# Kernel tuning notes

Measured on AMD Instinct MI355X. Metric: run time of the kernel, lower is better.

Reference implementation:

```python
import jax, jax.numpy as jnp
import numpy as np

BINS = 10

def setup_inputs() -> dict:
    key = jax.random.key(0)
    k1, k2 = jax.random.split(key)
    N, C = 131072, 1000
    pred = jax.random.normal(k1, (N, C), dtype=jnp.float32)
    target = jax.random.randint(k2, (N,), 0, C, dtype=jnp.int64)
    return {"pred": pred, "target": target}


def reference(pred, target):
    # edges = [0, 0.1, ..., 1.0]; last edge nudged so values_clip == 1.0 lands in last bin
    edges = jnp.arange(BINS + 1, dtype=pred.dtype) / BINS
    edges = edges.at[-1].add(1e-6)

    N = pred.shape[0]
    # per-sample cross entropy: -log_softmax(pred)[i, target[i]]
    log_probs = jax.nn.log_softmax(pred, axis=-1)          # [N, C]
    values = -jnp.take_along_axis(log_probs, target[:, None], axis=-1)[:, 0]  # [N]

    # detached, normalized gradient-magnitude proxy in [0, 1]
    values_clip = jax.lax.stop_gradient(values)
    values_clip = values_clip / jnp.max(values_clip)

    # histogram binning: inds = (vc >= edges[i]) & (vc < edges[i+1])
    bin_idx = jnp.searchsorted(edges, values_clip, side='right') - 1
    bin_idx = jnp.clip(bin_idx, 0, BINS - 1)
    counts = jnp.zeros((BINS,), dtype=pred.dtype).at[bin_idx].add(1.0)

    n_nonempty = jnp.sum(counts > 0).astype(pred.dtype)
    tot = jnp.asarray(N, dtype=pred.dtype)

    # weight per bin = tot / num_in_bin for occupied bins (empty bins never indexed)
    per_bin_w = tot / jnp.where(counts > 0, counts, 1.0)
    weights = per_bin_w[bin_idx] / jnp.maximum(n_nonempty, 1.0) / tot
    weights = jax.lax.stop_gradient(weights)

    return jnp.sum(weights * values)
```

## Files before the change

kernel.cpp:

```cpp
#include <hip/hip_runtime.h>

#define N_SAMPLES 131072
#define N_CLASSES 1000
#define BINS 10


__global__ __launch_bounds__(256) void values_kernel(const float* __restrict__ pred,
                                                     const int* __restrict__ target,
                                                     float* __restrict__ values) {
    const int wave = threadIdx.x >> 6;
    const int lane = threadIdx.x & 63;
    const int row = blockIdx.x * 4 + wave;
    if (row >= N_SAMPLES) return;

    const float4* __restrict__ rp = (const float4*)(pred + (size_t)row * N_CLASSES);

    float4 r0 = rp[lane];
    float4 r1 = rp[64 + lane];
    float4 r2 = rp[128 + lane];
    const int i3 = (192 + lane < 250) ? (192 + lane) : 249;
    float4 r3 = rp[i3];

    const int t = target[row];
    const float xt = pred[(size_t)row * N_CLASSES + t];

    const bool v3 = (192 + lane) < 250;
    const float NEG_INF = -INFINITY;
    float r3x = v3 ? r3.x : NEG_INF;
    float r3y = v3 ? r3.y : NEG_INF;
    float r3z = v3 ? r3.z : NEG_INF;
    float r3w = v3 ? r3.w : NEG_INF;

    float m0 = fmaxf(fmaxf(r0.x, r0.y), fmaxf(r0.z, r0.w));
    float m1 = fmaxf(fmaxf(r1.x, r1.y), fmaxf(r1.z, r1.w));
    float m2 = fmaxf(fmaxf(r2.x, r2.y), fmaxf(r2.z, r2.w));
    float m3 = fmaxf(fmaxf(r3x, r3y), fmaxf(r3z, r3w));
    float lmax = fmaxf(fmaxf(m0, m1), fmaxf(m2, m3));
#pragma unroll
    for (int off = 32; off > 0; off >>= 1)
        lmax = fmaxf(lmax, __shfl_xor(lmax, off, 64));

    float s0 = __expf(r0.x - lmax) + __expf(r0.y - lmax) +
               __expf(r0.z - lmax) + __expf(r0.w - lmax);
    float s1 = __expf(r1.x - lmax) + __expf(r1.y - lmax) +
               __expf(r1.z - lmax) + __expf(r1.w - lmax);
    float s2 = __expf(r2.x - lmax) + __expf(r2.y - lmax) +
               __expf(r2.z - lmax) + __expf(r2.w - lmax);
    float s3 = __expf(r3x - lmax) + __expf(r3y - lmax) +
               __expf(r3z - lmax) + __expf(r3w - lmax);
    float s = (s0 + s1) + (s2 + s3);
#pragma unroll
    for (int off = 32; off > 0; off >>= 1)
        s += __shfl_xor(s, off, 64);

    if (lane == 0)
        values[row] = logf(s) + lmax - xt;
}

__global__ __launch_bounds__(256) void max_kernel(const float* __restrict__ values,
                                                  unsigned int* __restrict__ vmax_bits) {
    __shared__ float smax[4];
    float m = 0.f;
    for (int i = blockIdx.x * blockDim.x + threadIdx.x; i < N_SAMPLES;
         i += gridDim.x * blockDim.x)
        m = fmaxf(m, values[i]);
#pragma unroll
    for (int off = 32; off > 0; off >>= 1)
        m = fmaxf(m, __shfl_xor(m, off, 64));
    if ((threadIdx.x & 63) == 0) smax[threadIdx.x >> 6] = m;
    __syncthreads();
    if (threadIdx.x == 0) {
        float bm = fmaxf(fmaxf(smax[0], smax[1]), fmaxf(smax[2], smax[3]));
        atomicMax(vmax_bits, __float_as_uint(bm));
    }
}

__global__ __launch_bounds__(256) void hist_kernel(const float* __restrict__ values,
                                                   const unsigned int* __restrict__ vmax_bits,
                                                   unsigned int* __restrict__ counts,
                                                   float* __restrict__ sums) {
    __shared__ unsigned int lc[BINS];
    __shared__ float ls[BINS];
    if (threadIdx.x < BINS) { lc[threadIdx.x] = 0u; ls[threadIdx.x] = 0.f; }
    __syncthreads();

    const float vmax = __uint_as_float(*vmax_bits);
    float edges[BINS + 1];
#pragma unroll
    for (int j = 0; j <= BINS; ++j) edges[j] = (float)j / 10.0f;
    edges[BINS] += 1e-6f;

    for (int i = blockIdx.x * blockDim.x + threadIdx.x; i < N_SAMPLES;
         i += gridDim.x * blockDim.x) {
        float v = values[i];
        float vc = v / vmax;
        int bin = -1;
#pragma unroll
        for (int j = 0; j <= BINS; ++j) bin += (edges[j] <= vc) ? 1 : 0;
        bin = min(max(bin, 0), BINS - 1);
        atomicAdd(&lc[bin], 1u);
        atomicAdd(&ls[bin], v);
    }
    __syncthreads();
    if (threadIdx.x < BINS) {
        if (lc[threadIdx.x]) {
            atomicAdd(&counts[threadIdx.x], lc[threadIdx.x]);
            atomicAdd(&sums[threadIdx.x], ls[threadIdx.x]);
        }
    }
}

__global__ void final_kernel(const unsigned int* __restrict__ counts,
                             const float* __restrict__ sums,
                             float* __restrict__ out) {
    if (threadIdx.x == 0 && blockIdx.x == 0) {
        int nn = 0;
        float acc = 0.f;
#pragma unroll
        for (int b = 0; b < BINS; ++b) {
            unsigned int c = counts[b];
            if (c > 0u) { ++nn; acc += sums[b] / (float)c; }
        }
        float nne = (nn > 0) ? (float)nn : 1.f;
        out[0] = acc / nne;
    }
}

extern "C" void kernel_launch(void* const* d_in, const int* in_sizes, int n_in,
                              void* d_out, int out_size, void* d_ws, size_t ws_size,
                              hipStream_t stream) {
    const float* pred = (const float*)d_in[0];
    const int* target = (const int*)d_in[1];
    float* out = (float*)d_out;

    float* values = (float*)d_ws;
    unsigned int* stats = (unsigned int*)((char*)d_ws + (size_t)N_SAMPLES * sizeof(float));
    unsigned int* counts = stats + 1;
    float* sums = (float*)(stats + 11);

    hipMemsetAsync(stats, 0, 21 * sizeof(unsigned int), stream);

    values_kernel<<<N_SAMPLES / 4, 256, 0, stream>>>(pred, target, values);
    max_kernel<<<256, 256, 0, stream>>>(values, stats);
    hist_kernel<<<256, 256, 0, stream>>>(values, stats, counts, sums);
    final_kernel<<<1, 64, 0, stream>>>(counts, sums, out);
}
```

Measured before the change: 669.2 us.

## Fuse max reduction into values kernel and finalize in last hist block

```diff
diff --git a/kernel.cpp b/kernel.cpp
--- a/kernel.cpp
+++ b/kernel.cpp
@@ -7,11 +7,12 @@
 
 __global__ __launch_bounds__(256) void values_kernel(const float* __restrict__ pred,
                                                      const int* __restrict__ target,
-                                                     float* __restrict__ values) {
+                                                     float* __restrict__ values,
+                                                     unsigned int* __restrict__ vmax_bits) {
+    __shared__ float smax[4];
     const int wave = threadIdx.x >> 6;
     const int lane = threadIdx.x & 63;
     const int row = blockIdx.x * 4 + wave;
-    if (row >= N_SAMPLES) return;
 
     const float4* __restrict__ rp = (const float4*)(pred + (size_t)row * N_CLASSES);
 
@@ -53,21 +54,11 @@
     for (int off = 32; off > 0; off >>= 1)
         s += __shfl_xor(s, off, 64);
 
-    if (lane == 0)
-        values[row] = logf(s) + lmax - xt;
-}
-
-__global__ __launch_bounds__(256) void max_kernel(const float* __restrict__ values,
-                                                  unsigned int* __restrict__ vmax_bits) {
-    __shared__ float smax[4];
-    float m = 0.f;
-    for (int i = blockIdx.x * blockDim.x + threadIdx.x; i < N_SAMPLES;
-         i += gridDim.x * blockDim.x)
-        m = fmaxf(m, values[i]);
-#pragma unroll
-    for (int off = 32; off > 0; off >>= 1)
-        m = fmaxf(m, __shfl_xor(m, off, 64));
-    if ((threadIdx.x & 63) == 0) smax[threadIdx.x >> 6] = m;
+    if (lane == 0) {
+        float val = logf(s) + lmax - xt;
+        values[row] = val;
+        smax[wave] = val;
+    }
     __syncthreads();
     if (threadIdx.x == 0) {
         float bm = fmaxf(fmaxf(smax[0], smax[1]), fmaxf(smax[2], smax[3]));
@@ -78,9 +69,12 @@
 __global__ __launch_bounds__(256) void hist_kernel(const float* __restrict__ values,
                                                    const unsigned int* __restrict__ vmax_bits,
                                                    unsigned int* __restrict__ counts,
-                                                   float* __restrict__ sums) {
+                                                   float* __restrict__ sums,
+                                                   unsigned int* __restrict__ done,
+                                                   float* __restrict__ out) {
     __shared__ unsigned int lc[BINS];
     __shared__ float ls[BINS];
+    __shared__ bool amLast;
     if (threadIdx.x < BINS) { lc[threadIdx.x] = 0u; ls[threadIdx.x] = 0.f; }
     __syncthreads();
 
@@ -108,18 +102,23 @@
             atomicAdd(&sums[threadIdx.x], ls[threadIdx.x]);
         }
     }
-}
 
-__global__ void final_kernel(const unsigned int* __restrict__ counts,
-                             const float* __restrict__ sums,
-                             float* __restrict__ out) {
-    if (threadIdx.x == 0 && blockIdx.x == 0) {
+    __syncthreads();
+    if (threadIdx.x == 0) {
+        __threadfence();
+        unsigned int ticket = atomicAdd(done, 1u);
+        amLast = (ticket == gridDim.x - 1);
+    }
+    __syncthreads();
+    if (amLast && threadIdx.x == 0) {
+        __threadfence();
         int nn = 0;
         float acc = 0.f;
 #pragma unroll
         for (int b = 0; b < BINS; ++b) {
-            unsigned int c = counts[b];
-            if (c > 0u) { ++nn; acc += sums[b] / (float)c; }
+            unsigned int c = atomicAdd(&counts[b], 0u);
+            float sm = atomicAdd(&sums[b], 0.0f);
+            if (c > 0u) { ++nn; acc += sm / (float)c; }
         }
         float nne = (nn > 0) ? (float)nn : 1.f;
         out[0] = acc / nne;
@@ -135,13 +134,13 @@
 
     float* values = (float*)d_ws;
     unsigned int* stats = (unsigned int*)((char*)d_ws + (size_t)N_SAMPLES * sizeof(float));
+    unsigned int* vmax_bits = stats;
     unsigned int* counts = stats + 1;
     float* sums = (float*)(stats + 11);
+    unsigned int* done = stats + 21;
 
-    hipMemsetAsync(stats, 0, 21 * sizeof(unsigned int), stream);
+    hipMemsetAsync(stats, 0, 22 * sizeof(unsigned int), stream);
 
-    values_kernel<<<N_SAMPLES / 4, 256, 0, stream>>>(pred, target, values);
-    max_kernel<<<256, 256, 0, stream>>>(values, stats);
-    hist_kernel<<<256, 256, 0, stream>>>(values, stats, counts, sums);
-    final_kernel<<<1, 64, 0, stream>>>(counts, sums, out);
+    values_kernel<<<N_SAMPLES / 4, 256, 0, stream>>>(pred, target, values, vmax_bits);
+    hist_kernel<<<256, 256, 0, stream>>>(values, vmax_bits, counts, sums, done, out);
 }
```

Measured after the change: 920.8 us. +37.6%, slower.
